# Kernel optimization log

Hardware: AMD Instinct MI355X
Metric: run time of the kernel (lower is better)

## Reference

```python
import jax, jax.numpy as jnp
import numpy as np

NUM_CLUSTERS = 32   # group label values lie in [0, 32)
EMB_DIM = 16
N_POINTS = 1_000_000
DELTA_DIST = 1.5
W_VAR, W_DIST, W_REG, W_SMOOTH, W_SEED = 3.0, 1.0, 0.001, 5.0, 5.0
LOG_CLAMP = -100.0  # torch BCELoss clamps log terms at -100


def setup_inputs() -> dict:
    key = jax.random.key(0)
    k1, k2, k3 = jax.random.split(key, 3)
    features = jax.random.normal(k1, (N_POINTS, EMB_DIM), dtype=jnp.float32)
    seediness = jax.random.normal(k2, (N_POINTS, 2), dtype=jnp.float32)
    group_labels = jax.random.randint(k3, (N_POINTS,), 0, NUM_CLUSTERS, dtype=jnp.int64)
    return {"features": features, "seediness": seediness, "group_labels": group_labels}


def _clustering_loss(features, seediness, labels):
    C = NUM_CLUSTERS
    N = features.shape[0]
    labels = labels.astype(jnp.int32)

    # --- cluster means (find_cluster_means) via segment reduce ---
    counts = jax.ops.segment_sum(jnp.ones((N,), features.dtype), labels, num_segments=C)  # [C]
    cmeans = jax.ops.segment_sum(features, labels, num_segments=C) / counts[:, None]      # [C, d]

    # --- per-cluster variance from seediness[:, 1] ---
    v = jnp.exp(seediness[:, 1])                                        # [N]
    var_c = jax.ops.segment_sum(v, labels, num_segments=C) / counts     # [C]

    # smoothness: mean over clusters of mean_i ((v_i - var_c)^2)
    sq_dev = (v - var_c[labels]) ** 2
    sm_c = jax.ops.segment_sum(sq_dev, labels, num_segments=C) / counts
    smoothness_loss = jnp.mean(sm_c)

    # --- squared distances from every point to every centroid: [N, C] ---
    f2 = jnp.sum(features * features, axis=1)          # [N]
    m2 = jnp.sum(cmeans * cmeans, axis=1)              # [C]
    D2 = jnp.maximum(f2[:, None] + m2[None, :] - 2.0 * (features @ cmeans.T), 0.0)

    logP = -D2 / (2.0 * var_c[None, :])                # log of prob map, [N, C]
    P = jnp.exp(logP)

    y = labels[:, None] == jnp.arange(C)[None, :]      # binary mask, [N, C]
    log_p = jnp.maximum(logP, LOG_CLAMP)
    log_1mp = jnp.maximum(jnp.log1p(-P), LOG_CLAMP)
    bce = -jnp.where(y, log_p, log_1mp)
    # var_loss = (1/C) * sum_c mean_i bce[i,c] == overall mean
    var_loss = jnp.mean(bce)

    # seediness target: prob of each point w.r.t. its own centroid (detached)
    seed_truth = jax.lax.stop_gradient(jnp.take_along_axis(P, labels[:, None], axis=1)[:, 0])
    seed_loss = jnp.mean((seed_truth - seediness[:, 0]) ** 2)

    # --- inter-cluster (distance) loss over centroid pairs ---
    diff2 = jnp.sum((cmeans[:, None, :] - cmeans[None, :, :]) ** 2, axis=-1)  # [C, C]
    eye = jnp.eye(C, dtype=bool)
    dd = jnp.sqrt(jnp.where(eye, 1.0, diff2))  # safe sqrt on diagonal
    hinge = jnp.maximum(2.0 * DELTA_DIST - dd, 0.0) ** 2
    dist_loss = jnp.sum(jnp.where(eye, 0.0, hinge)) / float((C - 1) * C)

    # --- regularization ---
    reg_loss = jnp.mean(jnp.sqrt(jnp.sum(cmeans * cmeans, axis=1)))

    loss = (W_VAR * var_loss + W_DIST * dist_loss + W_REG * reg_loss
            + W_SMOOTH * smoothness_loss + W_SEED * seed_loss)
    return loss


def reference(features, seediness, group_labels):
    return _clustering_loss(features, seediness, group_labels)
```

## Files before the change

### kernel.cpp

```cpp
#include <hip/hip_runtime.h>
#include <hip/hip_bf16.h>

#define NCLU 32
#define NDIM 16
#define W_VAR 3.0f
#define W_DIST 1.0f
#define W_REG 0.001f
#define W_SMOOTH 5.0f
#define W_SEED 5.0f

#define NBS 512
#define NBM 2048
#define SEG_STRIDE 640
#define PST     (NBS * SEG_STRIDE)
#define G_CM    (PST)
#define G_M2    (PST + 512)
#define G_IV    (PST + 544)
#define G_SMALL (PST + 576)
#define G_SUMS  (PST + 608)
#define PMAIN   (PST + 1280)

typedef __attribute__((ext_vector_type(8)))  short short8v;
typedef __attribute__((ext_vector_type(16))) float f32x16;

__device__ __forceinline__ short f2bf_rz(float x) {
    return (short)(__float_as_uint(x) >> 16);
}
__device__ __forceinline__ unsigned f2bf_rn_u(float x) {
    unsigned u = __float_as_uint(x);
    u += 0x7FFF + ((u >> 16) & 1);
    return u >> 16;
}

union BPack { short8v s8; unsigned u4[4]; __hip_bfloat162 h[4]; };

#define NW 4
__global__ __launch_bounds__(256)
void k_seg(const float* __restrict__ feat, const float* __restrict__ sd,
           const int* __restrict__ lab, float* __restrict__ ws, int n)
{
    __shared__ short sm[NW * 4096];
    int tid = threadIdx.x, wid = tid >> 6, lane = tid & 63;
    short* vt = sm + wid * 4096;
    short* yt = vt + 2048;
    int h0 = lane >> 5, m = lane & 31;
    int rowm = m * 64;
    int csig = (lane & 0x33) | ((lane & 4) << 1) | ((lane & 8) >> 1);

    {
        int4 z = {0, 0, 0, 0};
        int4* yz = (int4*)yt;
        yz[lane] = z; yz[lane + 64] = z; yz[lane + 128] = z; yz[lane + 192] = z;
        vt[18 * 64 + (csig ^ ((18 & 7) << 3))] = (short)0x3F80;
    }

    f32x16 acc = {};
    int nwin = (n + 63) >> 6;
    int wslot = blockIdx.x * NW + wid, nws = gridDim.x * NW;
    int prev = -1;

    for (int w = wslot; w < nwin; w += nws) {
        int p = w * 64 + lane;
        bool ok = (p < n);
        size_t pc = ok ? (size_t)p : (size_t)(n - 1);
        const float4* fp = (const float4*)(feat + pc * NDIM);
        float4 f0 = fp[0], f1 = fp[1], f2 = fp[2], f3 = fp[3];
        float sy = sd[2 * pc + 1];
        int lb = lab[pc];
        float v = __expf(sy);

        if (prev >= 0) yt[prev * 64 + (csig ^ ((prev & 7) << 3))] = 0;
        if (ok)        yt[lb * 64 + (csig ^ ((lb & 7) << 3))] = (short)0x3F80;
        prev = ok ? lb : -1;

        float ff[16] = { f0.x,f0.y,f0.z,f0.w, f1.x,f1.y,f1.z,f1.w,
                         f2.x,f2.y,f2.z,f2.w, f3.x,f3.y,f3.z,f3.w };
        #pragma unroll
        for (int j = 0; j < 16; ++j)
            vt[j * 64 + (csig ^ ((j & 7) << 3))] = f2bf_rz(ff[j]);
        vt[16 * 64 + (csig ^ ((16 & 7) << 3))] = (short)f2bf_rn_u(v);
        vt[17 * 64 + (csig ^ ((17 & 7) << 3))] = (short)f2bf_rn_u(v * v);

        #pragma unroll
        for (int q = 0; q < 4; ++q) {
            int o = rowm + ((8 * h0 + 16 * q) ^ ((m & 7) << 3));
            short8v A = *(short8v*)(vt + o);
            short8v B = *(short8v*)(yt + o);
            acc = __builtin_amdgcn_mfma_f32_32x32x16_bf16(A, B, acc, 0, 0, 0);
        }
    }

    __syncthreads();
    float* fsm = (float*)sm;
    #pragma unroll
    for (int r = 0; r < 16; ++r) fsm[wid * 1024 + lane * 16 + r] = acc[r];
    __syncthreads();
    for (int o = tid; o < NCLU * 19; o += 256) {
        int c = o / 19, j = o % 19;
        int hh = (j >> 2) & 1, r = (j & 3) + 4 * (j >> 3);
        int ln = c + 32 * hh;
        float s = 0.f;
        #pragma unroll
        for (int ww = 0; ww < NW; ++ww) s += fsm[ww * 1024 + ln * 16 + r];
        ws[(size_t)blockIdx.x * SEG_STRIDE + o] = s;
    }
}

__global__ __launch_bounds__(256)
void k_red1(float* __restrict__ ws)
{
    __shared__ float red[256];
    int tid = threadIdx.x;
    int o = blockIdx.x * 4 + (tid & 3);
    int brow = tid >> 2;
    float s = 0.f;
    #pragma unroll
    for (int k = 0; k < 8; ++k)
        s += ws[(size_t)(brow + 64 * k) * SEG_STRIDE + o];
    red[tid] = s;
    __syncthreads();
    for (int st = 128; st >= 4; st >>= 1) {
        if (tid < st) red[tid] += red[tid + st];
        __syncthreads();
    }
    if (tid < 4) ws[G_SUMS + blockIdx.x * 4 + tid] = red[tid];
}

__global__ __launch_bounds__(1024)
void k_stats(float* __restrict__ ws)
{
    __shared__ float sums[NCLU * 19];
    __shared__ float s_cm[NCLU * NDIM];
    __shared__ float red[1024];
    int tid = threadIdx.x;
    if (tid < NCLU * 19) sums[tid] = ws[G_SUMS + tid];
    __syncthreads();

    float contrib = 0.f;
    if (tid < NCLU) {
        int c = tid;
        float cnt = sums[c * 19 + 18];
        float inv = 1.0f / cnt;
        float var = sums[c * 19 + 16] * inv;
        float smo = sums[c * 19 + 17] * inv - var * var;
        float m2 = 0.f;
        for (int d = 0; d < NDIM; ++d) {
            float cm = sums[c * 19 + d] * inv;
            ws[G_CM + c * NDIM + d] = cm;
            s_cm[c * NDIM + d] = cm;
            m2 = fmaf(cm, cm, m2);
        }
        ws[G_M2 + c] = m2;
        ws[G_IV + c] = 0.5f / var;
        contrib = W_REG * sqrtf(m2) * (1.0f / NCLU) + W_SMOOTH * smo * (1.0f / NCLU);
    }
    __syncthreads();
    int i = tid >> 5, j = tid & 31;
    if (i != j) {
        float d2 = 0.f;
        for (int d = 0; d < NDIM; ++d) {
            float df = s_cm[i * NDIM + d] - s_cm[j * NDIM + d];
            d2 = fmaf(df, df, d2);
        }
        float dd = sqrtf(d2);
        float h = fmaxf(3.0f - dd, 0.f);
        contrib += W_DIST * h * h * (1.0f / ((NCLU - 1) * NCLU));
    }
    red[tid] = contrib;
    __syncthreads();
    for (int s = 512; s > 0; s >>= 1) {
        if (tid < s) red[tid] += red[tid + s];
        __syncthreads();
    }
    if (tid == 0) ws[G_SMALL] = red[0];
}

__global__ __launch_bounds__(256, 4)
void k_main(const float* __restrict__ feat, const float* __restrict__ sd,
            const int* __restrict__ lab, float* __restrict__ ws, int n)
{
    int tid = threadIdx.x, wid = tid >> 6, lane = tid & 63;
    int h0 = lane >> 5, pl = lane & 31;

    float iv = ws[G_IV + pl];
    float sc = iv * 1.44269504f;
    float m2 = ws[G_M2 + pl];
    const float* cmrow = ws + G_CM + pl * NDIM + 4 * h0;
    float4 ca = *(const float4*)(cmrow);
    float4 cb = *(const float4*)(cmrow + 8);
    float t2s = -2.0f * sc;
    BPack a1;
    a1.u4[0] = f2bf_rn_u(ca.x * t2s) | (f2bf_rn_u(ca.y * t2s) << 16);
    a1.u4[1] = f2bf_rn_u(ca.z * t2s) | (f2bf_rn_u(ca.w * t2s) << 16);
    a1.u4[2] = f2bf_rn_u(cb.x * t2s) | (f2bf_rn_u(cb.y * t2s) << 16);
    a1.u4[3] = f2bf_rn_u(cb.z * t2s) | (f2bf_rn_u(cb.w * t2s) << 16);
    BPack a2;
    a2.u4[0] = (h0 == 0) ? (f2bf_rn_u(m2 * sc) | (f2bf_rn_u(sc) << 16)) : 0u;
    a2.u4[1] = 0u; a2.u4[2] = 0u; a2.u4[3] = 0u;

    float bce = 0.f, sl = 0.f;
    int nt = (n + 31) >> 5;
    int slot = blockIdx.x * 4 + wid, nslots = gridDim.x * 4;

    for (int t = slot; t < nt; t += nslots) {
        int p = t * 32 + pl;
        bool ok = (p < n);
        size_t pc = ok ? (size_t)p : (size_t)(n - 1);
        const float* fr = feat + pc * NDIM + 4 * h0;
        float4 fa = *(const float4*)fr;
        float4 fb = *(const float4*)(fr + 8);
        int lb = lab[pc];
        float s0 = sd[2 * pc];

        float f2p = fa.x * fa.x;
        f2p = fmaf(fa.y, fa.y, f2p); f2p = fmaf(fa.z, fa.z, f2p);
        f2p = fmaf(fa.w, fa.w, f2p); f2p = fmaf(fb.x, fb.x, f2p);
        f2p = fmaf(fb.y, fb.y, f2p); f2p = fmaf(fb.z, fb.z, f2p);
        f2p = fmaf(fb.w, fb.w, f2p);
        float f2 = f2p + __shfl_xor(f2p, 32);

        BPack b1;
        float2 q01; q01.x = fa.x; q01.y = fa.y;
        float2 q23; q23.x = fa.z; q23.y = fa.w;
        float2 q45; q45.x = fb.x; q45.y = fb.y;
        float2 q67; q67.x = fb.z; q67.y = fb.w;
        b1.h[0] = __float22bfloat162_rn(q01);
        b1.h[1] = __float22bfloat162_rn(q23);
        b1.h[2] = __float22bfloat162_rn(q45);
        b1.h[3] = __float22bfloat162_rn(q67);
        BPack b2;
        b2.u4[0] = (h0 == 0) ? (0x3F80u | (f2bf_rn_u(f2) << 16)) : 0u;
        b2.u4[1] = 0u; b2.u4[2] = 0u; b2.u4[3] = 0u;

        f32x16 dz = {};
        f32x16 D = __builtin_amdgcn_mfma_f32_32x32x16_bf16(a1.s8, b1.s8, dz, 0, 0, 0);
        D = __builtin_amdgcn_mfma_f32_32x32x16_bf16(a2.s8, b2.s8, D, 0, 0, 0);

        int lb4 = lb - 4 * h0;
        unsigned ulb4 = (unsigned)lb4;
        bool hasown = (ulb4 < 32u) && ((ulb4 & 4u) == 0u);
        float bce_t = 0.f, ownP = 0.f;
        #pragma unroll
        for (int r = 0; r < 16; ++r) {
            const int CR = (r & 3) + 8 * (r >> 2);
            float q2 = fmaxf(D[r], 0.f);
            float P = __builtin_amdgcn_exp2f(-q2);
            float ts = fmaf(P * P, fmaf(P, fmaf(P, 0.25f, 0.33333333f), 0.5f), P);
            if (P > 0.5f) ts = -__logf(1.0f - P);
            bool own = (lb4 == CR);
            float contrib = fminf(own ? q2 * 0.69314718f : ts, 100.f);
            bce_t += contrib;
            ownP = own ? P : ownP;
        }
        float mask = ok ? 1.f : 0.f;
        bce = fmaf(mask, bce_t, bce);
        float e = ownP - s0;
        float smk = (hasown ? mask : 0.f);
        sl = fmaf(smk * e, e, sl);
    }

    __shared__ float rb[256], rsd[256];
    rb[tid] = bce; rsd[tid] = sl;
    __syncthreads();
    for (int s = 128; s > 0; s >>= 1) {
        if (tid < s) { rb[tid] += rb[tid + s]; rsd[tid] += rsd[tid + s]; }
        __syncthreads();
    }
    if (tid == 0) {
        float2 pr; pr.x = rb[0]; pr.y = rsd[0];
        ((float2*)(ws + PMAIN))[blockIdx.x] = pr;
    }
}

__global__ __launch_bounds__(1024)
void k_final(const float* __restrict__ ws, float* __restrict__ out, int n)
{
    __shared__ float rb[1024], rs[1024];
    int tid = threadIdx.x;
    float2 p0 = ((const float2*)(ws + PMAIN))[tid];
    float2 p1 = ((const float2*)(ws + PMAIN))[tid + 1024];
    rb[tid] = p0.x + p1.x; rs[tid] = p0.y + p1.y;
    __syncthreads();
    for (int s = 512; s > 0; s >>= 1) {
        if (tid < s) { rb[tid] += rb[tid + s]; rs[tid] += rs[tid + s]; }
        __syncthreads();
    }
    if (tid == 0) {
        float var_loss  = rb[0] / ((float)n * (float)NCLU);
        float seed_loss = rs[0] / (float)n;
        out[0] = W_VAR * var_loss + ws[G_SMALL] + W_SEED * seed_loss;
    }
}

extern "C" void kernel_launch(void* const* d_in, const int* in_sizes, int n_in,
                              void* d_out, int out_size, void* d_ws, size_t ws_size,
                              hipStream_t stream)
{
    const float* feat = (const float*)d_in[0];
    const float* sd   = (const float*)d_in[1];
    const int*   lab  = (const int*)d_in[2];
    float* ws = (float*)d_ws;
    int n = in_sizes[2];

    k_seg  <<<NBS, 256,  0, stream>>>(feat, sd, lab, ws, n);
    k_red1 <<<152, 256,  0, stream>>>(ws);
    k_stats<<<1,   1024, 0, stream>>>(ws);
    k_main <<<NBM, 256,  0, stream>>>(feat, sd, lab, ws, n);
    k_final<<<1,   1024, 0, stream>>>(ws, (float*)d_out, n);
}
```

Measured before the change: 53.92 us.

## Fuse reduction into stats kernel, prefetch next tile, fold f2 into MFMA

Merges the partial-sum reduction kernel into the stats kernel, so a single 1024-thread block now sums 512 block partials serially, which removes one launch. The main loop is software-pipelined: the next tile's features, labels and seediness are loaded while the current tile is computed. The cross-half shuffle for the squared norm is dropped by having each half contribute its partial norm through the second MFMA. The main grid shrinks to 1024 blocks and the final reducer to 512 threads. The serial 512-step reduction in one block may be slow.

```diff
diff --git a/kernel.cpp b/kernel.cpp
--- a/kernel.cpp
+++ b/kernel.cpp
@@ -10,14 +10,13 @@
 #define W_SEED 5.0f
 
 #define NBS 512
-#define NBM 2048
+#define NBM 1024
 #define SEG_STRIDE 640
 #define PST     (NBS * SEG_STRIDE)
 #define G_CM    (PST)
 #define G_M2    (PST + 512)
 #define G_IV    (PST + 544)
 #define G_SMALL (PST + 576)
-#define G_SUMS  (PST + 608)
 #define PMAIN   (PST + 1280)
 
 typedef __attribute__((ext_vector_type(8)))  short short8v;
@@ -106,34 +105,20 @@
     }
 }
 
-__global__ __launch_bounds__(256)
-void k_red1(float* __restrict__ ws)
-{
-    __shared__ float red[256];
-    int tid = threadIdx.x;
-    int o = blockIdx.x * 4 + (tid & 3);
-    int brow = tid >> 2;
-    float s = 0.f;
-    #pragma unroll
-    for (int k = 0; k < 8; ++k)
-        s += ws[(size_t)(brow + 64 * k) * SEG_STRIDE + o];
-    red[tid] = s;
-    __syncthreads();
-    for (int st = 128; st >= 4; st >>= 1) {
-        if (tid < st) red[tid] += red[tid + st];
-        __syncthreads();
-    }
-    if (tid < 4) ws[G_SUMS + blockIdx.x * 4 + tid] = red[tid];
-}
-
 __global__ __launch_bounds__(1024)
-void k_stats(float* __restrict__ ws)
+void k_redstats(float* __restrict__ ws)
 {
     __shared__ float sums[NCLU * 19];
     __shared__ float s_cm[NCLU * NDIM];
     __shared__ float red[1024];
     int tid = threadIdx.x;
-    if (tid < NCLU * 19) sums[tid] = ws[G_SUMS + tid];
+
+    if (tid < NCLU * 19) {
+        float s = 0.f;
+        #pragma unroll 8
+        for (int b = 0; b < NBS; ++b) s += ws[(size_t)b * SEG_STRIDE + tid];
+        sums[tid] = s;
+    }
     __syncthreads();
 
     float contrib = 0.f;
@@ -195,29 +180,45 @@
     a1.u4[2] = f2bf_rn_u(cb.x * t2s) | (f2bf_rn_u(cb.y * t2s) << 16);
     a1.u4[3] = f2bf_rn_u(cb.z * t2s) | (f2bf_rn_u(cb.w * t2s) << 16);
     BPack a2;
-    a2.u4[0] = (h0 == 0) ? (f2bf_rn_u(m2 * sc) | (f2bf_rn_u(sc) << 16)) : 0u;
+    a2.u4[0] = (h0 == 0) ? (f2bf_rn_u(m2 * sc) | (f2bf_rn_u(sc) << 16))
+                         : f2bf_rn_u(sc);
     a2.u4[1] = 0u; a2.u4[2] = 0u; a2.u4[3] = 0u;
 
     float bce = 0.f, sl = 0.f;
     int nt = (n + 31) >> 5;
     int slot = blockIdx.x * 4 + wid, nslots = gridDim.x * 4;
 
-    for (int t = slot; t < nt; t += nslots) {
-        int p = t * 32 + pl;
-        bool ok = (p < n);
-        size_t pc = ok ? (size_t)p : (size_t)(n - 1);
+    int t = slot;
+    bool live = (t < nt);
+    float4 fa = {}, fb = {};
+    int lb = 0; float s0 = 0.f;
+    if (live) {
+        size_t pc = (size_t)t * 32 + pl;
+        if (pc >= (size_t)n) pc = n - 1;
         const float* fr = feat + pc * NDIM + 4 * h0;
-        float4 fa = *(const float4*)fr;
-        float4 fb = *(const float4*)(fr + 8);
-        int lb = lab[pc];
-        float s0 = sd[2 * pc];
-
-        float f2p = fa.x * fa.x;
-        f2p = fmaf(fa.y, fa.y, f2p); f2p = fmaf(fa.z, fa.z, f2p);
-        f2p = fmaf(fa.w, fa.w, f2p); f2p = fmaf(fb.x, fb.x, f2p);
-        f2p = fmaf(fb.y, fb.y, f2p); f2p = fmaf(fb.z, fb.z, f2p);
-        f2p = fmaf(fb.w, fb.w, f2p);
-        float f2 = f2p + __shfl_xor(f2p, 32);
+        fa = *(const float4*)fr;
+        fb = *(const float4*)(fr + 8);
+        lb = lab[pc];
+        s0 = sd[2 * pc];
+    }
+
+    while (live) {
+        int tn = t + nslots;
+        bool nlive = (tn < nt);
+        int tc = nlive ? tn : 0;
+        size_t npc = (size_t)tc * 32 + pl;
+        if (npc >= (size_t)n) npc = n - 1;
+        const float* nfr = feat + npc * NDIM + 4 * h0;
+        float4 nfa = *(const float4*)nfr;
+        float4 nfb = *(const float4*)(nfr + 8);
+        int nlb = lab[npc];
+        float ns0 = sd[2 * npc];
+
+        float d0 = fmaf(fa.y, fa.y, fa.x * fa.x);
+        float d1 = fmaf(fa.w, fa.w, fa.z * fa.z);
+        float d2 = fmaf(fb.y, fb.y, fb.x * fb.x);
+        float d3 = fmaf(fb.w, fb.w, fb.z * fb.z);
+        float f2h = (d0 + d1) + (d2 + d3);
 
         BPack b1;
         float2 q01; q01.x = fa.x; q01.y = fa.y;
@@ -229,13 +230,16 @@
         b1.h[2] = __float22bfloat162_rn(q45);
         b1.h[3] = __float22bfloat162_rn(q67);
         BPack b2;
-        b2.u4[0] = (h0 == 0) ? (0x3F80u | (f2bf_rn_u(f2) << 16)) : 0u;
+        unsigned pk = f2bf_rn_u(f2h);
+        b2.u4[0] = (h0 == 0) ? (0x3F80u | (pk << 16)) : pk;
         b2.u4[1] = 0u; b2.u4[2] = 0u; b2.u4[3] = 0u;
 
         f32x16 dz = {};
         f32x16 D = __builtin_amdgcn_mfma_f32_32x32x16_bf16(a1.s8, b1.s8, dz, 0, 0, 0);
         D = __builtin_amdgcn_mfma_f32_32x32x16_bf16(a2.s8, b2.s8, D, 0, 0, 0);
 
+        int p = t * 32 + pl;
+        bool ok = (p < n);
         int lb4 = lb - 4 * h0;
         unsigned ulb4 = (unsigned)lb4;
         bool hasown = (ulb4 < 32u) && ((ulb4 & 4u) == 0u);
@@ -245,8 +249,11 @@
             const int CR = (r & 3) + 8 * (r >> 2);
             float q2 = fmaxf(D[r], 0.f);
             float P = __builtin_amdgcn_exp2f(-q2);
-            float ts = fmaf(P * P, fmaf(P, fmaf(P, 0.25f, 0.33333333f), 0.5f), P);
-            if (P > 0.5f) ts = -__logf(1.0f - P);
+            float s = fmaf(P, 0.25f, 0.33333333f);
+            s = fmaf(P, s, 0.5f);
+            float ser = fmaf(P * P, s, P);
+            float tl = -__logf(1.0f - P);
+            float ts = (P > 0.5f) ? tl : ser;
             bool own = (lb4 == CR);
             float contrib = fminf(own ? q2 * 0.69314718f : ts, 100.f);
             bce_t += contrib;
@@ -255,8 +262,11 @@
         float mask = ok ? 1.f : 0.f;
         bce = fmaf(mask, bce_t, bce);
         float e = ownP - s0;
-        float smk = (hasown ? mask : 0.f);
+        float smk = hasown ? mask : 0.f;
         sl = fmaf(smk * e, e, sl);
+
+        fa = nfa; fb = nfb; lb = nlb; s0 = ns0;
+        t = tn; live = nlive;
     }
 
     __shared__ float rb[256], rsd[256];
@@ -272,16 +282,16 @@
     }
 }
 
-__global__ __launch_bounds__(1024)
+__global__ __launch_bounds__(512)
 void k_final(const float* __restrict__ ws, float* __restrict__ out, int n)
 {
-    __shared__ float rb[1024], rs[1024];
+    __shared__ float rb[512], rs[512];
     int tid = threadIdx.x;
     float2 p0 = ((const float2*)(ws + PMAIN))[tid];
-    float2 p1 = ((const float2*)(ws + PMAIN))[tid + 1024];
+    float2 p1 = ((const float2*)(ws + PMAIN))[tid + 512];
     rb[tid] = p0.x + p1.x; rs[tid] = p0.y + p1.y;
     __syncthreads();
-    for (int s = 512; s > 0; s >>= 1) {
+    for (int s = 256; s > 0; s >>= 1) {
         if (tid < s) { rb[tid] += rb[tid + s]; rs[tid] += rs[tid + s]; }
         __syncthreads();
     }
@@ -302,9 +312,8 @@
     float* ws = (float*)d_ws;
     int n = in_sizes[2];
 
-    k_seg  <<<NBS, 256,  0, stream>>>(feat, sd, lab, ws, n);
-    k_red1 <<<152, 256,  0, stream>>>(ws);
-    k_stats<<<1,   1024, 0, stream>>>(ws);
-    k_main <<<NBM, 256,  0, stream>>>(feat, sd, lab, ws, n);
-    k_final<<<1,   1024, 0, stream>>>(ws, (float*)d_out, n);
-}
+    k_seg     <<<NBS, 256,  0, stream>>>(feat, sd, lab, ws, n);
+    k_redstats<<<1,   1024, 0, stream>>>(ws);
+    k_main    <<<NBM, 256,  0, stream>>>(feat, sd, lab, ws, n);
+    k_final   <<<1,   512,  0, stream>>>(ws, (float*)d_out, n);
+}
```

After: 75.82 us. +40.6%, slower.
